# Kernel tuning notes

Measured on AMD Instinct MI355X. Metric: run time of the kernel, lower is better.

## Reference

```python
import jax, jax.numpy as jnp
import numpy as np

K_SIZE = 5  # kernel_size


def _patches(f, k):
    # f: (b, c, h, w) -> (b, c, k*k, h, w), matching torch.nn.Unfold ordering
    # (patch positions row-major (kh, kw) per channel), padding = k//2, stride 1.
    p = k // 2
    b, c, h, w = f.shape
    fp = jnp.pad(f, ((0, 0), (0, 0), (p, p), (p, p)))
    slices = [fp[:, :, i:i + h, j:j + w] for i in range(k) for j in range(k)]
    return jnp.stack(slices, axis=2)


def _conv1x1(w, b, f):
    # w: (out, in), b: (out,), f: (b, in, h, w)
    return jnp.einsum('oc,bchw->bohw', w, f) + b[None, :, None, None]


def setup_inputs() -> dict:
    key = jax.random.key(0)
    ks = jax.random.split(key, 8)
    B, XC, YC, FT, H, W = 4, 64, 64, 64, 128, 128
    x = jax.random.normal(ks[0], (B, XC, H, W), dtype=jnp.float32)
    y = jax.random.normal(ks[1], (B, YC, H, W), dtype=jnp.float32)
    sx = 1.0 / np.sqrt(XC)
    sy = 1.0 / np.sqrt(YC)
    sf = 1.0 / np.sqrt(FT)
    wx = jax.random.uniform(ks[2], (FT, XC), jnp.float32, -sx, sx)
    bx = jax.random.uniform(ks[3], (FT,), jnp.float32, -sx, sx)
    wy = jax.random.uniform(ks[4], (FT, YC), jnp.float32, -sy, sy)
    by = jax.random.uniform(ks[5], (FT,), jnp.float32, -sy, sy)
    wo = jax.random.uniform(ks[6], (XC, FT), jnp.float32, -sf, sf)
    bo = jax.random.uniform(ks[7], (XC,), jnp.float32, -sf, sf)
    return {"x": x, "y": y, "wx": wx, "bx": bx, "wy": wy, "by": by, "wo": wo, "bo": bo}


def reference(x, y, wx, bx, wy, by, wo, bo):
    k = K_SIZE
    q = _conv1x1(wy, by, y)            # (b, feat, h, w): Q (the q axis of size 1 is squeezed)
    Kp = _patches(q, k)                # (b, feat, k^2, h, w): unfold(conv_y(y))
    v = _conv1x1(wx, bx, x)            # (b, feat, h, w)
    Vp = _patches(v, k)                # (b, feat, k^2, h, w): unfold(conv_x(x))
    A = jnp.einsum('bckhw,bchw->bkhw', Kp, q)   # scores over k^2 neighbors
    A = jax.nn.softmax(A, axis=1)               # softmax over dim=1 (k^2)
    out = jnp.einsum('bkhw,bckhw->bchw', A, Vp)  # aggregate values
    out = _conv1x1(wo, bo, out)
    return out + x
```

## Files before the change

kernel.cpp:

```cpp
#include <hip/hip_runtime.h>

#define HH   128
#define WW   128
#define HW   (HH * WW)
#define CC   64
#define TILE 8
#define HALO 12
#define NHP  (HALO * HALO)

typedef unsigned int uint32;
typedef _Float16 h2   __attribute__((ext_vector_type(2)));
typedef __fp16   h2b  __attribute__((ext_vector_type(2)));
typedef _Float16 h8   __attribute__((ext_vector_type(8)));
typedef float    f32x4 __attribute__((ext_vector_type(4)));

__device__ __forceinline__ uint32 pkrtz(float a, float b) {
    h2b r = __builtin_amdgcn_cvt_pkrtz(a, b);
    return __builtin_bit_cast(uint32, r);
}
__device__ __forceinline__ float dot2(uint32 a, uint32 b, float c) {
#if __has_builtin(__builtin_amdgcn_fdot2)
    return __builtin_amdgcn_fdot2(__builtin_bit_cast(h2b, a),
                                  __builtin_bit_cast(h2b, b), c, false);
#else
    h2 x = __builtin_bit_cast(h2, a), y = __builtin_bit_cast(h2, b);
    return c + (float)x.x * (float)y.x + (float)x.y * (float)y.y;
#endif
}
__device__ __forceinline__ f32x4 mfma16(uint4 a, uint4 b, f32x4 c) {
    return __builtin_amdgcn_mfma_f32_16x16x32_f16(
        __builtin_bit_cast(h8, a), __builtin_bit_cast(h8, b), c, 0, 0, 0);
}
__device__ __forceinline__ uint4 pack_w8(const float* __restrict__ w) {
    const float4 lo = *(const float4*)w;
    const float4 hi = *(const float4*)(w + 4);
    uint4 r;
    r.x = pkrtz(lo.x, lo.y); r.y = pkrtz(lo.z, lo.w);
    r.z = pkrtz(hi.x, hi.y); r.w = pkrtz(hi.z, hi.w);
    return r;
}

__global__ __launch_bounds__(256, 4)
void fused_attn(const float* __restrict__ x, const float* __restrict__ y,
                const float* __restrict__ wx, const float* __restrict__ bx,
                const float* __restrict__ wy, const float* __restrict__ by,
                const float* __restrict__ wo, const float* __restrict__ bo,
                float* __restrict__ out)
{
    __shared__ uint32 Ah[NHP * 32];
    __shared__ uint32 Bh[NHP * 32];

    const int lin  = blockIdx.x;
    const int xcd  = lin & 7;
    const int rr   = lin >> 3;
    const int b    = xcd >> 1;
    const int half = xcd & 1;
    const int ty0  = (((rr >> 4) + half * 8)) * TILE;
    const int tx0  = (rr & 15) * TILE;

    const int t = threadIdx.x;

    for (int i = t; i < NHP * 8; i += 256) {
        const int c   = i / NHP;
        const int pix = i - c * NHP;
        const int hy  = pix / HALO, hx = pix - hy * HALO;
        int gy = ty0 + hy - 2, gx = tx0 + hx - 2;
        const bool ok = ((unsigned)gy < HH) & ((unsigned)gx < WW);
        if (!ok) { gy = 0; gx = 0; }
        const size_t base = (size_t)b * CC * HW + (size_t)(c * 8) * HW
                          + (size_t)gy * WW + gx;
        float yv[8], xv[8];
        #pragma unroll
        for (int j = 0; j < 8; ++j) {
            yv[j] = y[base + (size_t)j * HW];
            xv[j] = x[base + (size_t)j * HW];
        }
        uint4 yq, xq;
        yq.x = pkrtz(yv[0], yv[1]); yq.y = pkrtz(yv[2], yv[3]);
        yq.z = pkrtz(yv[4], yv[5]); yq.w = pkrtz(yv[6], yv[7]);
        xq.x = pkrtz(xv[0], xv[1]); xq.y = pkrtz(xv[2], xv[3]);
        xq.z = pkrtz(xv[4], xv[5]); xq.w = pkrtz(xv[6], xv[7]);
        const int w0 = (c ^ (pix & 7)) * 4;
        *(uint4*)&Ah[pix * 32 + w0] = yq;
        *(uint4*)&Bh[pix * 32 + w0] = xq;
    }
    __syncthreads();

    const int wv = t >> 6;
    const int ln = t & 63;
    const int lm = ln & 15;
    const int qd = ln >> 4;
    const int chunk = wv * 2 + (qd >> 1);

    {
        const uint4 aq0 = pack_w8(wy + (wv * 16 + lm) * CC + qd * 8);
        const uint4 aq1 = pack_w8(wy + (wv * 16 + lm) * CC + qd * 8 + 32);
        f32x4 accq[9];
        #pragma unroll
        for (int nt = 0; nt < 9; ++nt) {
            const int px = nt * 16 + lm, sw = px & 7;
            const uint4 b0 = *(const uint4*)&Ah[px * 32 + ((qd    ) ^ sw) * 4];
            const uint4 b1 = *(const uint4*)&Ah[px * 32 + ((qd + 4) ^ sw) * 4];
            f32x4 a = {0.f, 0.f, 0.f, 0.f};
            a = mfma16(aq0, b0, a); a = mfma16(aq1, b1, a); accq[nt] = a;
        }
        __syncthreads();
        const float4 bq = *(const float4*)(by + wv * 16 + qd * 4);
        #pragma unroll
        for (int nt = 0; nt < 9; ++nt) {
            const int px = nt * 16 + lm;
            const int hy = px / HALO, hx = px - hy * HALO;
            const int gy = ty0 + hy - 2, gx = tx0 + hx - 2;
            uint2 wq = {0u, 0u};
            if (((unsigned)gy < HH) & ((unsigned)gx < WW)) {
                wq.x = pkrtz(accq[nt].x + bq.x, accq[nt].y + bq.y);
                wq.y = pkrtz(accq[nt].z + bq.z, accq[nt].w + bq.w);
            }
            *(uint2*)&Ah[px * 32 + (chunk ^ (px & 7)) * 4 + (qd & 1) * 2] = wq;
        }
    }

    uint2 xres[4];
    {
        const uint4 av0 = pack_w8(wx + (wv * 16 + lm) * CC + qd * 8);
        const uint4 av1 = pack_w8(wx + (wv * 16 + lm) * CC + qd * 8 + 32);
        f32x4 accv[9];
        #pragma unroll
        for (int nt = 0; nt < 9; ++nt) {
            const int px = nt * 16 + lm, sw = px & 7;
            const uint4 c0 = *(const uint4*)&Bh[px * 32 + ((qd    ) ^ sw) * 4];
            const uint4 c1 = *(const uint4*)&Bh[px * 32 + ((qd + 4) ^ sw) * 4];
            f32x4 v = {0.f, 0.f, 0.f, 0.f};
            v = mfma16(av0, c0, v); v = mfma16(av1, c1, v); accv[nt] = v;
        }
        #pragma unroll
        for (int nt = 0; nt < 4; ++nt) {
            const int px = nt * 16 + lm;
            const int hpix = ((px >> 3) + 2) * HALO + (px & 7) + 2;
            xres[nt] = *(const uint2*)
                &Bh[hpix * 32 + (chunk ^ (hpix & 7)) * 4 + (qd & 1) * 2];
        }
        __syncthreads();
        const float4 bv = *(const float4*)(bx + wv * 16 + qd * 4);
        #pragma unroll
        for (int nt = 0; nt < 9; ++nt) {
            const int px = nt * 16 + lm;
            const int hy = px / HALO, hx = px - hy * HALO;
            const int gy = ty0 + hy - 2, gx = tx0 + hx - 2;
            uint2 wvv = {0u, 0u};
            if (((unsigned)gy < HH) & ((unsigned)gx < WW)) {
                wvv.x = pkrtz(accv[nt].x + bv.x, accv[nt].y + bv.y);
                wvv.y = pkrtz(accv[nt].z + bv.z, accv[nt].w + bv.w);
            }
            *(uint2*)&Bh[px * 32 + (chunk ^ (px & 7)) * 4 + (qd & 1) * 2] = wvv;
        }
    }

    const int p    = t >> 2, sub = t & 3;
    const int py   = p >> 3, px8 = p & 7;
    const int crow = (py + 2) * HALO + (px8 + 2);

    uint32 qc[8];
    {
        const int c0 = ((2 * sub) ^ (crow & 7)) * 4;
        const int c1 = ((2 * sub + 1) ^ (crow & 7)) * 4;
        *(uint4*)&qc[0] = *(const uint4*)&Ah[crow * 32 + c0];
        *(uint4*)&qc[4] = *(const uint4*)&Ah[crow * 32 + c1];
    }

    float sc[25];
    #pragma unroll
    for (int dy = 0; dy < 5; ++dy)
        #pragma unroll
        for (int dx = 0; dx < 5; ++dx) {
            const int nrow = (py + dy) * HALO + (px8 + dx);
            const int c0 = ((2 * sub) ^ (nrow & 7)) * 4;
            const int c1 = ((2 * sub + 1) ^ (nrow & 7)) * 4;
            const uint4 r0 = *(const uint4*)&Ah[nrow * 32 + c0];
            const uint4 r1 = *(const uint4*)&Ah[nrow * 32 + c1];
            float s = 0.f;
            s = dot2(qc[0], r0.x, s); s = dot2(qc[1], r0.y, s);
            s = dot2(qc[2], r0.z, s); s = dot2(qc[3], r0.w, s);
            s = dot2(qc[4], r1.x, s); s = dot2(qc[5], r1.y, s);
            s = dot2(qc[6], r1.z, s); s = dot2(qc[7], r1.w, s);
            s += __shfl_xor(s, 1);
            s += __shfl_xor(s, 2);
            sc[dy * 5 + dx] = s;
        }

    float mx = sc[0];
    #pragma unroll
    for (int k = 1; k < 25; ++k) mx = fmaxf(mx, sc[k]);
    float sum = 0.f;
    #pragma unroll
    for (int k = 0; k < 25; ++k) { sc[k] = __expf(sc[k] - mx); sum += sc[k]; }
    const float inv = 1.f / sum;

    __syncthreads();

    h2 ag[8];
    #pragma unroll
    for (int k = 0; k < 8; ++k) ag[k] = (h2)(_Float16)0;
    #pragma unroll
    for (int dy = 0; dy < 5; ++dy)
        #pragma unroll
        for (int dx = 0; dx < 5; ++dx) {
            const int nrow = (py + dy) * HALO + (px8 + dx);
            const int c0 = ((2 * sub) ^ (nrow & 7)) * 4;
            const int c1 = ((2 * sub + 1) ^ (nrow & 7)) * 4;
            const uint4 r0 = *(const uint4*)&Bh[nrow * 32 + c0];
            const uint4 r1 = *(const uint4*)&Bh[nrow * 32 + c1];
            const _Float16 af = (_Float16)sc[dy * 5 + dx];
            const h2 a2 = {af, af};
            ag[0] += a2 * __builtin_bit_cast(h2, r0.x);
            ag[1] += a2 * __builtin_bit_cast(h2, r0.y);
            ag[2] += a2 * __builtin_bit_cast(h2, r0.z);
            ag[3] += a2 * __builtin_bit_cast(h2, r0.w);
            ag[4] += a2 * __builtin_bit_cast(h2, r1.x);
            ag[5] += a2 * __builtin_bit_cast(h2, r1.y);
            ag[6] += a2 * __builtin_bit_cast(h2, r1.z);
            ag[7] += a2 * __builtin_bit_cast(h2, r1.w);
        }

    __syncthreads();
    {
        const _Float16 ih = (_Float16)inv;
        const h2 i2 = {ih, ih};
        #pragma unroll
        for (int k = 0; k < 8; ++k) ag[k] *= i2;
        const int c0 = ((2 * sub) ^ (p & 7)) * 4;
        const int c1 = ((2 * sub + 1) ^ (p & 7)) * 4;
        uint4 w0, w1;
        w0.x = __builtin_bit_cast(uint32, ag[0]); w0.y = __builtin_bit_cast(uint32, ag[1]);
        w0.z = __builtin_bit_cast(uint32, ag[2]); w0.w = __builtin_bit_cast(uint32, ag[3]);
        w1.x = __builtin_bit_cast(uint32, ag[4]); w1.y = __builtin_bit_cast(uint32, ag[5]);
        w1.z = __builtin_bit_cast(uint32, ag[6]); w1.w = __builtin_bit_cast(uint32, ag[7]);
        *(uint4*)&Ah[p * 32 + c0] = w0;
        *(uint4*)&Ah[p * 32 + c1] = w1;
    }
    __syncthreads();

    {
        const uint4 a0 = pack_w8(wo + (wv * 16 + lm) * CC + qd * 8);
        const uint4 a1 = pack_w8(wo + (wv * 16 + lm) * CC + qd * 8 + 32);
        const float4 bq = *(const float4*)(bo + wv * 16 + qd * 4);
        #pragma unroll
        for (int nt = 0; nt < 4; ++nt) {
            const int px = nt * 16 + lm, sw = px & 7;
            const uint4 b0 = *(const uint4*)&Ah[px * 32 + ((qd    ) ^ sw) * 4];
            const uint4 b1 = *(const uint4*)&Ah[px * 32 + ((qd + 4) ^ sw) * 4];
            f32x4 a = {0.f, 0.f, 0.f, 0.f};
            a = mfma16(a0, b0, a);
            a = mfma16(a1, b1, a);
            const int gh = ty0 + (px >> 3), gw = tx0 + (px & 7);
            const h2 xp0 = __builtin_bit_cast(h2, xres[nt].x);
            const h2 xp1 = __builtin_bit_cast(h2, xres[nt].y);
            const float rv[4] = {(float)xp0.x, (float)xp0.y,
                                 (float)xp1.x, (float)xp1.y};
            const float av4[4] = {a.x + bq.x, a.y + bq.y, a.z + bq.z, a.w + bq.w};
            #pragma unroll
            for (int r = 0; r < 4; ++r) {
                const int oc = wv * 16 + qd * 4 + r;
                const size_t ad = (size_t)(b * CC + oc) * HW + (size_t)gh * WW + gw;
                out[ad] = av4[r] + rv[r];
            }
        }
    }
}

extern "C" void kernel_launch(void* const* d_in, const int* in_sizes, int n_in,
                              void* d_out, int out_size, void* d_ws, size_t ws_size,
                              hipStream_t stream) {
    const float* x  = (const float*)d_in[0];
    const float* y  = (const float*)d_in[1];
    const float* wx = (const float*)d_in[2];
    const float* bx = (const float*)d_in[3];
    const float* wy = (const float*)d_in[4];
    const float* by = (const float*)d_in[5];
    const float* wo = (const float*)d_in[6];
    const float* bo = (const float*)d_in[7];
    float* out = (float*)d_out;
    (void)d_ws; (void)ws_size;

    fused_attn<<<dim3(1024), 256, 0, stream>>>(x, y, wx, bx, wy, by, wo, bo, out);
}
```

Measured before the change: 119.5 us.

## Reuse one LDS buffer for Q and V phases to double occupancy

Drops the second shared buffer so Q and V share one halo buffer. The y tile is staged, projected and scored first, then the x tile is loaded and projected into the same buffer. This halves LDS per block so launch bounds can rise to 8 blocks per CU. In exchange the x load can no longer overlap the y load, extra barriers are added, and the softmax normalisation moves into the per-neighbour weight before aggregation.

```diff
diff --git a/kernel.cpp b/kernel.cpp
--- a/kernel.cpp
+++ b/kernel.cpp
@@ -40,7 +40,7 @@
     return r;
 }
 
-__global__ __launch_bounds__(256, 4)
+__global__ __launch_bounds__(256, 8)
 void fused_attn(const float* __restrict__ x, const float* __restrict__ y,
                 const float* __restrict__ wx, const float* __restrict__ bx,
                 const float* __restrict__ wy, const float* __restrict__ by,
@@ -48,7 +48,6 @@
                 float* __restrict__ out)
 {
     __shared__ uint32 Ah[NHP * 32];
-    __shared__ uint32 Bh[NHP * 32];
 
     const int lin  = blockIdx.x;
     const int xcd  = lin & 7;
@@ -59,38 +58,37 @@
     const int tx0  = (rr & 15) * TILE;
 
     const int t = threadIdx.x;
-
-    for (int i = t; i < NHP * 8; i += 256) {
-        const int c   = i / NHP;
-        const int pix = i - c * NHP;
-        const int hy  = pix / HALO, hx = pix - hy * HALO;
-        int gy = ty0 + hy - 2, gx = tx0 + hx - 2;
-        const bool ok = ((unsigned)gy < HH) & ((unsigned)gx < WW);
-        if (!ok) { gy = 0; gx = 0; }
-        const size_t base = (size_t)b * CC * HW + (size_t)(c * 8) * HW
-                          + (size_t)gy * WW + gx;
-        float yv[8], xv[8];
-        #pragma unroll
-        for (int j = 0; j < 8; ++j) {
-            yv[j] = y[base + (size_t)j * HW];
-            xv[j] = x[base + (size_t)j * HW];
-        }
-        uint4 yq, xq;
-        yq.x = pkrtz(yv[0], yv[1]); yq.y = pkrtz(yv[2], yv[3]);
-        yq.z = pkrtz(yv[4], yv[5]); yq.w = pkrtz(yv[6], yv[7]);
-        xq.x = pkrtz(xv[0], xv[1]); xq.y = pkrtz(xv[2], xv[3]);
-        xq.z = pkrtz(xv[4], xv[5]); xq.w = pkrtz(xv[6], xv[7]);
-        const int w0 = (c ^ (pix & 7)) * 4;
-        *(uint4*)&Ah[pix * 32 + w0] = yq;
-        *(uint4*)&Bh[pix * 32 + w0] = xq;
-    }
-    __syncthreads();
+    const size_t bbase = (size_t)b * CC * HW;
 
     const int wv = t >> 6;
     const int ln = t & 63;
     const int lm = ln & 15;
     const int qd = ln >> 4;
     const int chunk = wv * 2 + (qd >> 1);
+
+#define STAGE_ONE(src, ii)                                                    \
+    {                                                                         \
+        const int c   = (ii) / NHP;                                           \
+        const int pix = (ii) - c * NHP;                                       \
+        const int hy  = pix / HALO, hx = pix - hy * HALO;                     \
+        int gy = ty0 + hy - 2, gx = tx0 + hx - 2;                             \
+        const bool ok = ((unsigned)gy < HH) & ((unsigned)gx < WW);            \
+        if (!ok) { gy = 0; gx = 0; }                                          \
+        const size_t base = bbase + (size_t)(c * 8) * HW                      \
+                          + (size_t)gy * WW + gx;                             \
+        float v8[8];                                                          \
+        _Pragma("unroll")                                                     \
+        for (int j = 0; j < 8; ++j) v8[j] = (src)[base + (size_t)j * HW];     \
+        uint4 pq;                                                             \
+        pq.x = pkrtz(v8[0], v8[1]); pq.y = pkrtz(v8[2], v8[3]);               \
+        pq.z = pkrtz(v8[4], v8[5]); pq.w = pkrtz(v8[6], v8[7]);               \
+        *(uint4*)&Ah[pix * 32 + (c ^ (pix & 7)) * 4] = pq;                    \
+    }
+
+    #pragma unroll
+    for (int r = 0; r < 4; ++r) { STAGE_ONE(y, t + r * 256) }
+    if (t < NHP * 8 - 1024) { STAGE_ONE(y, t + 1024) }
+    __syncthreads();
 
     {
         const uint4 aq0 = pack_w8(wy + (wv * 16 + lm) * CC + qd * 8);
@@ -119,6 +117,52 @@
             *(uint2*)&Ah[px * 32 + (chunk ^ (px & 7)) * 4 + (qd & 1) * 2] = wq;
         }
     }
+    __syncthreads();
+
+    const int p    = t >> 2, sub = t & 3;
+    const int py   = p >> 3, px8 = p & 7;
+    const int crow = (py + 2) * HALO + (px8 + 2);
+
+    float sc[25];
+    {
+        uint32 qc[8];
+        const int c0 = ((2 * sub) ^ (crow & 7)) * 4;
+        const int c1 = ((2 * sub + 1) ^ (crow & 7)) * 4;
+        *(uint4*)&qc[0] = *(const uint4*)&Ah[crow * 32 + c0];
+        *(uint4*)&qc[4] = *(const uint4*)&Ah[crow * 32 + c1];
+        #pragma unroll
+        for (int dy = 0; dy < 5; ++dy)
+            #pragma unroll
+            for (int dx = 0; dx < 5; ++dx) {
+                const int nrow = (py + dy) * HALO + (px8 + dx);
+                const int n0 = ((2 * sub) ^ (nrow & 7)) * 4;
+                const int n1 = ((2 * sub + 1) ^ (nrow & 7)) * 4;
+                const uint4 r0 = *(const uint4*)&Ah[nrow * 32 + n0];
+                const uint4 r1 = *(const uint4*)&Ah[nrow * 32 + n1];
+                float s = 0.f;
+                s = dot2(qc[0], r0.x, s); s = dot2(qc[1], r0.y, s);
+                s = dot2(qc[2], r0.z, s); s = dot2(qc[3], r0.w, s);
+                s = dot2(qc[4], r1.x, s); s = dot2(qc[5], r1.y, s);
+                s = dot2(qc[6], r1.z, s); s = dot2(qc[7], r1.w, s);
+                s += __shfl_xor(s, 1);
+                s += __shfl_xor(s, 2);
+                sc[dy * 5 + dx] = s;
+            }
+    }
+    float mx = sc[0];
+    #pragma unroll
+    for (int k = 1; k < 25; ++k) mx = fmaxf(mx, sc[k]);
+    float sum = 0.f;
+    #pragma unroll
+    for (int k = 0; k < 25; ++k) { sc[k] = __expf(sc[k] - mx); sum += sc[k]; }
+    const float inv = 1.f / sum;
+    __syncthreads();
+
+    #pragma unroll
+    for (int r = 0; r < 4; ++r) { STAGE_ONE(x, t + r * 256) }
+    if (t < NHP * 8 - 1024) { STAGE_ONE(x, t + 1024) }
+#undef STAGE_ONE
+    __syncthreads();
 
     uint2 xres[4];
     {
@@ -128,8 +172,8 @@
         #pragma unroll
         for (int nt = 0; nt < 9; ++nt) {
             const int px = nt * 16 + lm, sw = px & 7;
-            const uint4 c0 = *(const uint4*)&Bh[px * 32 + ((qd    ) ^ sw) * 4];
-            const uint4 c1 = *(const uint4*)&Bh[px * 32 + ((qd + 4) ^ sw) * 4];
+            const uint4 c0 = *(const uint4*)&Ah[px * 32 + ((qd    ) ^ sw) * 4];
+            const uint4 c1 = *(const uint4*)&Ah[px * 32 + ((qd + 4) ^ sw) * 4];
             f32x4 v = {0.f, 0.f, 0.f, 0.f};
             v = mfma16(av0, c0, v); v = mfma16(av1, c1, v); accv[nt] = v;
         }
@@ -138,7 +182,7 @@
             const int px = nt * 16 + lm;
             const int hpix = ((px >> 3) + 2) * HALO + (px & 7) + 2;
             xres[nt] = *(const uint2*)
-                &Bh[hpix * 32 + (chunk ^ (hpix & 7)) * 4 + (qd & 1) * 2];
+                &Ah[hpix * 32 + (chunk ^ (hpix & 7)) * 4 + (qd & 1) * 2];
         }
         __syncthreads();
         const float4 bv = *(const float4*)(bx + wv * 16 + qd * 4);
@@ -152,23 +196,14 @@
                 wvv.x = pkrtz(accv[nt].x + bv.x, accv[nt].y + bv.y);
                 wvv.y = pkrtz(accv[nt].z + bv.z, accv[nt].w + bv.w);
             }
-            *(uint2*)&Bh[px * 32 + (chunk ^ (px & 7)) * 4 + (qd & 1) * 2] = wvv;
-        }
-    }
-
-    const int p    = t >> 2, sub = t & 3;
-    const int py   = p >> 3, px8 = p & 7;
-    const int crow = (py + 2) * HALO + (px8 + 2);
-
-    uint32 qc[8];
-    {
-        const int c0 = ((2 * sub) ^ (crow & 7)) * 4;
-        const int c1 = ((2 * sub + 1) ^ (crow & 7)) * 4;
-        *(uint4*)&qc[0] = *(const uint4*)&Ah[crow * 32 + c0];
-        *(uint4*)&qc[4] = *(const uint4*)&Ah[crow * 32 + c1];
-    }
-
-    float sc[25];
+            *(uint2*)&Ah[px * 32 + (chunk ^ (px & 7)) * 4 + (qd & 1) * 2] = wvv;
+        }
+    }
+    __syncthreads();
+
+    h2 ag[8];
+    #pragma unroll
+    for (int k = 0; k < 8; ++k) ag[k] = (h2)(_Float16)0;
     #pragma unroll
     for (int dy = 0; dy < 5; ++dy)
         #pragma unroll
@@ -178,39 +213,7 @@
             const int c1 = ((2 * sub + 1) ^ (nrow & 7)) * 4;
             const uint4 r0 = *(const uint4*)&Ah[nrow * 32 + c0];
             const uint4 r1 = *(const uint4*)&Ah[nrow * 32 + c1];
-            float s = 0.f;
-            s = dot2(qc[0], r0.x, s); s = dot2(qc[1], r0.y, s);
-            s = dot2(qc[2], r0.z, s); s = dot2(qc[3], r0.w, s);
-            s = dot2(qc[4], r1.x, s); s = dot2(qc[5], r1.y, s);
-            s = dot2(qc[6], r1.z, s); s = dot2(qc[7], r1.w, s);
-            s += __shfl_xor(s, 1);
-            s += __shfl_xor(s, 2);
-            sc[dy * 5 + dx] = s;
-        }
-
-    float mx = sc[0];
-    #pragma unroll
-    for (int k = 1; k < 25; ++k) mx = fmaxf(mx, sc[k]);
-    float sum = 0.f;
-    #pragma unroll
-    for (int k = 0; k < 25; ++k) { sc[k] = __expf(sc[k] - mx); sum += sc[k]; }
-    const float inv = 1.f / sum;
-
-    __syncthreads();
-
-    h2 ag[8];
-    #pragma unroll
-    for (int k = 0; k < 8; ++k) ag[k] = (h2)(_Float16)0;
-    #pragma unroll
-    for (int dy = 0; dy < 5; ++dy)
-        #pragma unroll
-        for (int dx = 0; dx < 5; ++dx) {
-            const int nrow = (py + dy) * HALO + (px8 + dx);
-            const int c0 = ((2 * sub) ^ (nrow & 7)) * 4;
-            const int c1 = ((2 * sub + 1) ^ (nrow & 7)) * 4;
-            const uint4 r0 = *(const uint4*)&Bh[nrow * 32 + c0];
-            const uint4 r1 = *(const uint4*)&Bh[nrow * 32 + c1];
-            const _Float16 af = (_Float16)sc[dy * 5 + dx];
+            const _Float16 af = (_Float16)(sc[dy * 5 + dx] * inv);
             const h2 a2 = {af, af};
             ag[0] += a2 * __builtin_bit_cast(h2, r0.x);
             ag[1] += a2 * __builtin_bit_cast(h2, r0.y);
@@ -221,13 +224,8 @@
             ag[6] += a2 * __builtin_bit_cast(h2, r1.z);
             ag[7] += a2 * __builtin_bit_cast(h2, r1.w);
         }
-
-    __syncthreads();
-    {
-        const _Float16 ih = (_Float16)inv;
-        const h2 i2 = {ih, ih};
-        #pragma unroll
-        for (int k = 0; k < 8; ++k) ag[k] *= i2;
+    __syncthreads();
+    {
         const int c0 = ((2 * sub) ^ (p & 7)) * 4;
         const int c1 = ((2 * sub + 1) ^ (p & 7)) * 4;
         uint4 w0, w1;
```

After: 179.8 us. 1.5x slower.
